# Kernel optimization log

Hardware: AMD Instinct MI355X
Metric: run time of the kernel (lower is better)

Reference implementation:

```python
import jax, jax.numpy as jnp
import numpy as np

N_NODES = 50000
N_EDGES = 800000
D = 64  # in_dim == hidden_dim == out_dim
BN_EPS = 1e-5


def setup_inputs() -> dict:
    key = jax.random.key(0)
    ks = jax.random.split(key, 12)
    x = jax.random.normal(ks[0], (N_NODES, D), dtype=jnp.float32)
    edge_index = jax.random.randint(ks[1], (2, N_EDGES), 0, N_NODES, dtype=jnp.int64)
    scale = 1.0 / np.sqrt(D)
    W1 = jax.random.normal(ks[2], (D, D), dtype=jnp.float32) * scale
    b1 = jnp.zeros((D,), jnp.float32)
    W2 = jax.random.normal(ks[3], (D, D), dtype=jnp.float32) * scale
    b2 = jnp.zeros((D,), jnp.float32)
    W3 = jax.random.normal(ks[4], (D, D), dtype=jnp.float32) * scale
    b3 = jnp.zeros((D,), jnp.float32)
    # BatchNorm (eval mode: running stats) params for the two hidden layers
    g1 = jnp.ones((D,), jnp.float32); be1 = jnp.zeros((D,), jnp.float32)
    m1 = jax.random.normal(ks[5], (D,), dtype=jnp.float32) * 0.1
    v1 = jax.random.uniform(ks[6], (D,), dtype=jnp.float32, minval=0.5, maxval=1.5)
    g2 = jnp.ones((D,), jnp.float32); be2 = jnp.zeros((D,), jnp.float32)
    m2 = jax.random.normal(ks[7], (D,), dtype=jnp.float32) * 0.1
    v2 = jax.random.uniform(ks[8], (D,), dtype=jnp.float32, minval=0.5, maxval=1.5)
    return {"x": x, "edge_index": edge_index,
            "W1": W1, "b1": b1, "g1": g1, "be1": be1, "m1": m1, "v1": v1,
            "W2": W2, "b2": b2, "g2": g2, "be2": be2, "m2": m2, "v2": v2,
            "W3": W3, "b3": b3}


def reference(x, edge_index, W1, b1, g1, be1, m1, v1,
              W2, b2, g2, be2, m2, v2, W3, b3):
    N = x.shape[0]
    loop = jnp.arange(N, dtype=edge_index.dtype)
    src = jnp.concatenate([edge_index[0], loop])  # [E+N]
    dst = jnp.concatenate([edge_index[1], loop])
    # GCN symmetric normalization: deg over dst (with self loops)
    deg = jax.ops.segment_sum(jnp.ones(dst.shape, x.dtype), dst, num_segments=N)
    dinv = jnp.where(deg > 0, jax.lax.rsqrt(deg), 0.0)
    norm = (dinv[src] * dinv[dst])[:, None]  # [E+N, 1]

    def gcn_conv(h, W, b):
        h = h @ W  # linear transform first (PyG GCNConv order)
        return jax.ops.segment_sum(h[src] * norm, dst, num_segments=N) + b

    def bn(h, g, be, m, v):  # eval-mode BatchNorm1d
        return (h - m) * jax.lax.rsqrt(v + BN_EPS) * g + be

    h = jax.nn.relu(bn(gcn_conv(x, W1, b1), g1, be1, m1, v1))
    h = jax.nn.relu(bn(gcn_conv(h, W2, b2), g2, be2, m2, v2))
    return gcn_conv(h, W3, b3)
```

## Files before the change

kernel.cpp:

```cpp
#include <hip/hip_runtime.h>
#include <hip/hip_fp16.h>

#define D 64
#define BN_EPS 1e-5f
typedef unsigned short u16;
typedef unsigned int u32;

#define NB_MAX 256
#define A3_EDGES 4096
#define BCHUNK 5120

__global__ __launch_bounds__(256) void k_setup(
    const void* __restrict__ ei, int N, int* __restrict__ flag,
    int* __restrict__ bucketCur,
    const float* __restrict__ g1, const float* __restrict__ be1,
    const float* __restrict__ m1, const float* __restrict__ v1,
    const float* __restrict__ g2, const float* __restrict__ be2,
    const float* __restrict__ m2, const float* __restrict__ v2,
    float* __restrict__ bn, __half* __restrict__ rowzA, __half* __restrict__ rowzB) {
    int d = threadIdx.x;
    bucketCur[d] = 0;
    if (d < 64) {
        float s = g1[d] * rsqrtf(v1[d] + BN_EPS);
        bn[d] = s; bn[64 + d] = be1[d] - m1[d] * s;
        float q = g2[d] * rsqrtf(v2[d] + BN_EPS);
        bn[128 + d] = q; bn[192 + d] = be2[d] - m2[d] * q;
    } else if (d == 64) {
        const long long* p = (const long long*)ei;
        int ok = 1;
        for (int j = 0; j < 16; ++j) {
            long long v = p[j];
            if (v < 0 || v >= (long long)N) { ok = 0; break; }
        }
        *flag = ok;
    }
    if (d >= 128 && d < 160) {
        ((u32*)rowzA)[d - 128] = 0;
        ((u32*)rowzB)[d - 128] = 0;
    }
}

__device__ __forceinline__ int get_idx(const void* ei, int is64, int pos) {
    if (is64) return (int)((const long long*)ei)[pos];
    return ((const int*)ei)[pos];
}

__global__ __launch_bounds__(256) void k_bucket_scatter(
    const void* __restrict__ ei, const int* __restrict__ flag, int E, int nb,
    int* __restrict__ bucketCur, u32* __restrict__ staged) {
    __shared__ u32 recs[A3_EDGES];
    __shared__ int hist[NB_MAX];
    __shared__ int lpos[NB_MAX];
    __shared__ int gbase[NB_MAX];
    const int tid = threadIdx.x;
    const int base = blockIdx.x * A3_EDGES;
    const int cnt = min(A3_EDGES, E - base);
    const int is64 = *flag;
    for (int i = tid; i < nb; i += 256) hist[i] = 0;
    __syncthreads();
    u32 myrec[16];
    const int per = (cnt + 255) >> 8;
    for (int j = 0; j < per; ++j) {
        int o = j * 256 + tid;
        if (o < cnt) {
            int e = base + o;
            u32 src = (u32)get_idx(ei, is64, e);
            u32 dst = (u32)get_idx(ei, is64, E + e);
            u32 bkt = dst >> 8;
            myrec[j] = (bkt << 24) | (src << 8) | (dst & 255u);
            atomicAdd(&hist[bkt], 1);
        } else myrec[j] = 0xffffffffu;
    }
    __syncthreads();
    int v = (tid < nb) ? hist[tid] : 0;
    lpos[tid] = v; __syncthreads();
    for (int off = 1; off < 256; off <<= 1) {
        int t = (tid >= off) ? lpos[tid - off] : 0;
        __syncthreads(); lpos[tid] += t; __syncthreads();
    }
    int excl = lpos[tid] - v;
    if (tid < nb && v > 0) gbase[tid] = atomicAdd(&bucketCur[tid], v);
    __syncthreads();
    if (tid < nb) { lpos[tid] = excl; hist[tid] = 0; }
    __syncthreads();
    for (int j = 0; j < per; ++j) {
        u32 r = myrec[j];
        if (r != 0xffffffffu) {
            int b = (int)(r >> 24);
            int p = lpos[b] + atomicAdd(&hist[b], 1);
            recs[p] = r;
        }
    }
    __syncthreads();
    const int wave = tid >> 6, lane = tid & 63;
    for (int b = wave; b < nb; b += 4) {
        int c = hist[b]; if (!c) continue;
        int gb = gbase[b];
        int lsrc = lpos[b];
        for (int k = lane; k < c; k += 64) {
            int gp = gb + k;
            if (gp < BCHUNK)
                staged[(size_t)b * BCHUNK + gp] = recs[lsrc + k];
        }
    }
}

__global__ __launch_bounds__(256) void k_bucket_build(
    const u32* __restrict__ staged, const int* __restrict__ bucketCur,
    int2* __restrict__ rowbc, float* __restrict__ dinv, u16* __restrict__ csr,
    int N) {
    __shared__ int hist[256], off[256], cur[256];
    const int b = blockIdx.x, tid = threadIdx.x;
    const int beg = b * BCHUNK;
    const int cnt = min(bucketCur[b], BCHUNK);
    const int end = beg + cnt;
    hist[tid] = 0;
    __syncthreads();
    for (int i = beg + tid; i < end; i += 256)
        atomicAdd(&hist[staged[i] & 255u], 1);
    __syncthreads();
    int v = hist[tid];
    off[tid] = v; __syncthreads();
    for (int o = 1; o < 256; o <<= 1) {
        int t = (tid >= o) ? off[tid - o] : 0;
        __syncthreads(); off[tid] += t; __syncthreads();
    }
    int excl = off[tid] - v;
    const int dst = b * 256 + tid;
    if (dst < N) {
        rowbc[dst] = make_int2(beg + excl, v);
        dinv[dst] = rsqrtf(1.0f + (float)v);
    }
    __syncthreads();
    off[tid] = excl; cur[tid] = 0;
    __syncthreads();
    for (int i = beg + tid; i < end; i += 256) {
        u32 r = staged[i];
        int dl = (int)(r & 255u);
        int p = beg + off[dl] + atomicAdd(&cur[dl], 1);
        csr[p] = (u16)((r >> 8) & 0xffffu);
    }
}

#define GROWS 64
__global__ __launch_bounds__(256) void k_gemm(
    const float* __restrict__ h, const float* __restrict__ W,
    const float* __restrict__ dinv, __half* __restrict__ h2s, int N) {
    __shared__ float hs[GROWS * 65];
    __shared__ float Ws[64 * 64];
    const int tid = threadIdx.x;
    const int row0 = blockIdx.x * GROWS;
    const int nrow = min(GROWS, N - row0);
    const float4* Wp = (const float4*)W;
    float4* Wsp = (float4*)Ws;
    for (int i = tid; i < 1024; i += 256) Wsp[i] = Wp[i];
    const float4* hp = (const float4*)h + (size_t)row0 * 16;
    for (int i = tid; i < nrow * 16; i += 256) {
        float4 t = hp[i];
        int r = i >> 4, c4 = (i & 15) << 2;
        float* dp = &hs[r * 65 + c4];
        dp[0] = t.x; dp[1] = t.y; dp[2] = t.z; dp[3] = t.w;
    }
    __syncthreads();
    const int r = tid >> 2, q = tid & 3;
    const int row = row0 + r;
    if (r >= nrow) return;
    float out[16];
#pragma unroll
    for (int c = 0; c < 16; ++c) out[c] = 0.f;
    for (int k = 0; k < 64; ++k) {
        float a = hs[r * 65 + k];
        const float* Wk = &Ws[k * 64 + q * 16];
#pragma unroll
        for (int c = 0; c < 16; ++c) out[c] = fmaf(a, Wk[c], out[c]);
    }
    const float di = dinv[row];
    u32 pk[8];
#pragma unroll
    for (int c = 0; c < 8; ++c) {
        u32 lo = __half_as_ushort(__float2half(di * out[2 * c]));
        u32 hi = __half_as_ushort(__float2half(di * out[2 * c + 1]));
        pk[c] = (hi << 16) | lo;
    }
    uint4* op = (uint4*)(h2s + (size_t)row * 64 + q * 16);
    op[0] = make_uint4(pk[0], pk[1], pk[2], pk[3]);
    op[1] = make_uint4(pk[4], pk[5], pk[6], pk[7]);
}

__device__ __forceinline__ void acc8(float* acc, const float4& v) {
    const __half2* hv = (const __half2*)&v;
#pragma unroll
    for (int q2 = 0; q2 < 4; ++q2) {
        float2 t = __half22float2(hv[q2]);
        acc[2 * q2] += t.x; acc[2 * q2 + 1] += t.y;
    }
}

__device__ __forceinline__ float4 pk4(float4 a, const float4& b) {
    __half2* ha = (__half2*)&a;
    const __half2* hb = (const __half2*)&b;
#pragma unroll
    for (int i = 0; i < 4; ++i) ha[i] = __hadd2(ha[i], hb[i]);
    return a;
}

template <int MODE>
__global__ __launch_bounds__(256) void k_gather(
    const int2* __restrict__ rowbc, const u16* __restrict__ csr,
    const __half* __restrict__ h2s, const float* __restrict__ dinv,
    const float* __restrict__ b, const float* __restrict__ bn, int bn_off,
    const float* __restrict__ Wn, __half* __restrict__ h2o,
    float* __restrict__ outp, int N) {
    __shared__ float ytile[16][68];
    const int tid = threadIdx.x;
    const int lane = tid & 63;
    const int n16 = tid >> 4;
    const int node = blockIdx.x * 16 + n16;
    const int g2 = (lane >> 3) & 1;
    const int f = lane & 7;
    const int lbase = lane & ~15;
    const int l16 = lane & 15;
    const bool valid = node < N;

    float acc[8];
#pragma unroll
    for (int k = 0; k < 8; ++k) acc[k] = 0.f;

    if (valid) {
        int2 bc = rowbc[node];
        const int beg = bc.x, end = bc.x + bc.y;
        float4 sv = ((const float4*)(h2s + (size_t)node * 64))[f];
        if (g2 == 0) acc8(acc, sv);

        for (int c = beg; c < end; c += 16) {
            int p = c + l16;
            int idx = (p < end) ? (int)csr[p] : N;
            float4 v[8];
#pragma unroll
            for (int j = 0; j < 8; ++j) {
                int s = __shfl(idx, lbase + 2 * j + g2);
                v[j] = ((const float4*)(h2s + (size_t)s * 64))[f];
            }
            float4 t0 = pk4(v[0], v[1]), t1 = pk4(v[2], v[3]);
            float4 t2 = pk4(v[4], v[5]), t3 = pk4(v[6], v[7]);
            t0 = pk4(t0, t1); t2 = pk4(t2, t3);
            t0 = pk4(t0, t2);
            acc8(acc, t0);
        }
#pragma unroll
        for (int k = 0; k < 8; ++k) acc[k] += __shfl_xor(acc[k], 8);

        if (g2 == 0) {
            const float dn = dinv[node];
            float bb[8], y[8];
            ((float4*)bb)[0] = ((const float4*)b)[2 * f];
            ((float4*)bb)[1] = ((const float4*)b)[2 * f + 1];
#pragma unroll
            for (int k = 0; k < 8; ++k) y[k] = dn * acc[k] + bb[k];
            if (MODE == 0) {
                float ss[8], tt[8];
                ((float4*)ss)[0] = ((const float4*)(bn + bn_off))[2 * f];
                ((float4*)ss)[1] = ((const float4*)(bn + bn_off))[2 * f + 1];
                ((float4*)tt)[0] = ((const float4*)(bn + bn_off + 64))[2 * f];
                ((float4*)tt)[1] = ((const float4*)(bn + bn_off + 64))[2 * f + 1];
#pragma unroll
                for (int k = 0; k < 8; ++k) y[k] = fmaxf(y[k] * ss[k] + tt[k], 0.f);
                float4* yt = (float4*)&ytile[n16][f * 8];
                yt[0] = make_float4(y[0], y[1], y[2], y[3]);
                yt[1] = make_float4(y[4], y[5], y[6], y[7]);
            } else {
                float4* op = (float4*)(outp + (size_t)node * 64 + f * 8);
                op[0] = make_float4(y[0], y[1], y[2], y[3]);
                op[1] = make_float4(y[4], y[5], y[6], y[7]);
            }
        }
    }
    if (MODE == 0) {
        __syncthreads();
        if (valid) {
            const int cq = (tid & 15) << 2;
            float z0 = 0.f, z1 = 0.f, z2 = 0.f, z3 = 0.f;
#pragma unroll 4
            for (int k = 0; k < 64; ++k) {
                float a = ytile[n16][k];
                float4 w = *(const float4*)(Wn + k * 64 + cq);
                z0 = fmaf(a, w.x, z0); z1 = fmaf(a, w.y, z1);
                z2 = fmaf(a, w.z, z2); z3 = fmaf(a, w.w, z3);
            }
            const float dn = dinv[node];
            u32 p0 = ((u32)__half_as_ushort(__float2half(dn * z1)) << 16)
                   | __half_as_ushort(__float2half(dn * z0));
            u32 p1 = ((u32)__half_as_ushort(__float2half(dn * z3)) << 16)
                   | __half_as_ushort(__float2half(dn * z2));
            *(uint2*)(h2o + (size_t)node * 64 + cq) = make_uint2(p0, p1);
        }
    }
}

extern "C" void kernel_launch(void* const* d_in, const int* in_sizes, int n_in,
                              void* d_out, int out_size, void* d_ws, size_t ws_size,
                              hipStream_t stream) {
    const float* x  = (const float*)d_in[0];
    const void*  ei = d_in[1];
    const float* W1 = (const float*)d_in[2];
    const float* b1 = (const float*)d_in[3];
    const float* g1 = (const float*)d_in[4];
    const float* be1= (const float*)d_in[5];
    const float* m1 = (const float*)d_in[6];
    const float* v1 = (const float*)d_in[7];
    const float* W2 = (const float*)d_in[8];
    const float* b2 = (const float*)d_in[9];
    const float* g2 = (const float*)d_in[10];
    const float* be2= (const float*)d_in[11];
    const float* m2 = (const float*)d_in[12];
    const float* v2 = (const float*)d_in[13];
    const float* W3 = (const float*)d_in[14];
    const float* b3 = (const float*)d_in[15];

    const int N = in_sizes[0] / D;
    const int E = in_sizes[1] / 2;
    const int nb = (N + 255) >> 8;
    float* out = (float*)d_out;

    char* ws = (char*)d_ws;
    int*   flag      = (int*)ws;
    float* bn        = (float*)(ws + 256);
    int*   bucketCur = (int*)(ws + 2048);
    int2*  rowbc     = (int2*)(ws + 8192);
    float* dinv      = (float*)(ws + 8192 + (size_t)N * 8 + 64);
    u32*   staged    = (u32*)((char*)dinv + (size_t)N * 4 + 192);
    u16*   csr       = (u16*)((char*)staged + (size_t)nb * BCHUNK * 4 + 256);
    __half* bufA     = (__half*)((char*)csr + (size_t)nb * BCHUNK * 2 + 256);
    __half* bufC     = bufA + (size_t)(N + 1) * D;

    const int gGemm = (N + GROWS - 1) / GROWS;
    const int gGath = (N + 15) / 16;
    const int gA3   = (E + A3_EDGES - 1) / A3_EDGES;

    k_setup<<<1, 256, 0, stream>>>(ei, N, flag, bucketCur,
                                   g1, be1, m1, v1, g2, be2, m2, v2, bn,
                                   bufA + (size_t)N * D, bufC + (size_t)N * D);
    k_bucket_scatter<<<gA3, 256, 0, stream>>>(ei, flag, E, nb, bucketCur, staged);
    k_bucket_build<<<nb, 256, 0, stream>>>(staged, bucketCur, rowbc, dinv, csr, N);

    k_gemm<<<gGemm, 256, 0, stream>>>(x, W1, dinv, bufA, N);
    k_gather<0><<<gGath, 256, 0, stream>>>(rowbc, csr, bufA, dinv, b1, bn, 0,
                                           W2, bufC, nullptr, N);
    k_gather<0><<<gGath, 256, 0, stream>>>(rowbc, csr, bufC, dinv, b2, bn, 128,
                                           W3, bufA, nullptr, N);
    k_gather<1><<<gGath, 256, 0, stream>>>(rowbc, csr, bufA, dinv, b3, bn, 0,
                                           nullptr, nullptr, out, N);
}
```

Before: 161.4 us.

## Halve scatter chunk, widen bucket build to 512 threads, use nontemporal gathers

Halves the edges per bucket-scatter block so there are twice as many blocks and a smaller per-thread record array. Runs the bucket-build kernel with 512 threads, guarding the 256-entry histogram and scan so more threads stream the staged edges. In the gather kernels, neighbor row loads become nontemporal vector loads, meant to reduce cache pollution during the random gathers. The risk is that nontemporal hints lower L2 reuse of rows that are fetched many times, and the smaller scatter chunks mean more global atomics on the bucket counters.

Result: slower. 200.8 us (+24.4%).

```diff
diff --git a/kernel.cpp b/kernel.cpp
--- a/kernel.cpp
+++ b/kernel.cpp
@@ -5,9 +5,10 @@
 #define BN_EPS 1e-5f
 typedef unsigned short u16;
 typedef unsigned int u32;
+typedef float __attribute__((ext_vector_type(4))) f32x4;
 
 #define NB_MAX 256
-#define A3_EDGES 4096
+#define A3_EDGES 2048
 #define BCHUNK 5120
 
 __global__ __launch_bounds__(256) void k_setup(
@@ -58,7 +59,7 @@
     const int is64 = *flag;
     for (int i = tid; i < nb; i += 256) hist[i] = 0;
     __syncthreads();
-    u32 myrec[16];
+    u32 myrec[8];
     const int per = (cnt + 255) >> 8;
     for (int j = 0; j < per; ++j) {
         int o = j * 256 + tid;
@@ -105,7 +106,7 @@
     }
 }
 
-__global__ __launch_bounds__(256) void k_bucket_build(
+__global__ __launch_bounds__(512) void k_bucket_build(
     const u32* __restrict__ staged, const int* __restrict__ bucketCur,
     int2* __restrict__ rowbc, float* __restrict__ dinv, u16* __restrict__ csr,
     int N) {
@@ -114,27 +115,32 @@
     const int beg = b * BCHUNK;
     const int cnt = min(bucketCur[b], BCHUNK);
     const int end = beg + cnt;
-    hist[tid] = 0;
-    __syncthreads();
-    for (int i = beg + tid; i < end; i += 256)
+    if (tid < 256) hist[tid] = 0;
+    __syncthreads();
+    for (int i = beg + tid; i < end; i += 512)
         atomicAdd(&hist[staged[i] & 255u], 1);
     __syncthreads();
-    int v = hist[tid];
-    off[tid] = v; __syncthreads();
+    int v = 0;
+    if (tid < 256) { v = hist[tid]; off[tid] = v; }
+    __syncthreads();
     for (int o = 1; o < 256; o <<= 1) {
-        int t = (tid >= o) ? off[tid - o] : 0;
-        __syncthreads(); off[tid] += t; __syncthreads();
-    }
-    int excl = off[tid] - v;
-    const int dst = b * 256 + tid;
-    if (dst < N) {
-        rowbc[dst] = make_int2(beg + excl, v);
-        dinv[dst] = rsqrtf(1.0f + (float)v);
-    }
-    __syncthreads();
-    off[tid] = excl; cur[tid] = 0;
-    __syncthreads();
-    for (int i = beg + tid; i < end; i += 256) {
+        int t = 0;
+        if (tid < 256 && tid >= o) t = off[tid - o];
+        __syncthreads();
+        if (tid < 256) off[tid] += t;
+        __syncthreads();
+    }
+    if (tid < 256) {
+        int excl = off[tid] - v;
+        const int dst = b * 256 + tid;
+        if (dst < N) {
+            rowbc[dst] = make_int2(beg + excl, v);
+            dinv[dst] = rsqrtf(1.0f + (float)v);
+        }
+        off[tid] = excl; cur[tid] = 0;
+    }
+    __syncthreads();
+    for (int i = beg + tid; i < end; i += 512) {
         u32 r = staged[i];
         int dl = (int)(r & 255u);
         int p = beg + off[dl] + atomicAdd(&cur[dl], 1);
@@ -187,7 +193,7 @@
     op[1] = make_uint4(pk[4], pk[5], pk[6], pk[7]);
 }
 
-__device__ __forceinline__ void acc8(float* acc, const float4& v) {
+__device__ __forceinline__ void acc8(float* acc, const f32x4& v) {
     const __half2* hv = (const __half2*)&v;
 #pragma unroll
     for (int q2 = 0; q2 < 4; ++q2) {
@@ -196,7 +202,7 @@
     }
 }
 
-__device__ __forceinline__ float4 pk4(float4 a, const float4& b) {
+__device__ __forceinline__ f32x4 pk4(f32x4 a, const f32x4& b) {
     __half2* ha = (__half2*)&a;
     const __half2* hb = (const __half2*)&b;
 #pragma unroll
@@ -229,20 +235,21 @@
     if (valid) {
         int2 bc = rowbc[node];
         const int beg = bc.x, end = bc.x + bc.y;
-        float4 sv = ((const float4*)(h2s + (size_t)node * 64))[f];
+        f32x4 sv = *((const f32x4*)(h2s + (size_t)node * 64) + f);
         if (g2 == 0) acc8(acc, sv);
 
         for (int c = beg; c < end; c += 16) {
             int p = c + l16;
             int idx = (p < end) ? (int)csr[p] : N;
-            float4 v[8];
+            f32x4 v[8];
 #pragma unroll
             for (int j = 0; j < 8; ++j) {
                 int s = __shfl(idx, lbase + 2 * j + g2);
-                v[j] = ((const float4*)(h2s + (size_t)s * 64))[f];
+                v[j] = __builtin_nontemporal_load(
+                    (const f32x4*)(h2s + (size_t)s * 64) + f);
             }
-            float4 t0 = pk4(v[0], v[1]), t1 = pk4(v[2], v[3]);
-            float4 t2 = pk4(v[4], v[5]), t3 = pk4(v[6], v[7]);
+            f32x4 t0 = pk4(v[0], v[1]), t1 = pk4(v[2], v[3]);
+            f32x4 t2 = pk4(v[4], v[5]), t3 = pk4(v[6], v[7]);
             t0 = pk4(t0, t1); t2 = pk4(t2, t3);
             t0 = pk4(t0, t2);
             acc8(acc, t0);
@@ -341,7 +348,7 @@
                                    g1, be1, m1, v1, g2, be2, m2, v2, bn,
                                    bufA + (size_t)N * D, bufC + (size_t)N * D);
     k_bucket_scatter<<<gA3, 256, 0, stream>>>(ei, flag, E, nb, bucketCur, staged);
-    k_bucket_build<<<nb, 256, 0, stream>>>(staged, bucketCur, rowbc, dinv, csr, N);
+    k_bucket_build<<<nb, 512, 0, stream>>>(staged, bucketCur, rowbc, dinv, csr, N);
 
     k_gemm<<<gGemm, 256, 0, stream>>>(x, W1, dinv, bufA, N);
     k_gather<0><<<gGath, 256, 0, stream>>>(rowbc, csr, bufA, dinv, b1, bn, 0,
```
